# Kernel optimization log

Hardware: AMD Instinct MI355X
Metric: run time of the kernel (lower is better)

The kernel has to match this reference:

```python
import jax, jax.numpy as jnp
import numpy as np
from jax import lax

NPOINT, RADIUS, NSAMPLE = 1024, 0.2, 32
MLP = [64, 64, 128]
EPS = 1e-5  # BatchNorm eps


def setup_inputs() -> dict:
    key = jax.random.key(0)
    ks = jax.random.split(key, 16)
    B, N, D = 16, 4096, 64
    inp = {
        "xyz": jax.random.uniform(ks[0], (B, 3, N), jnp.float32),   # points in unit cube
        "points": jax.random.normal(ks[1], (B, D, N), jnp.float32),  # per-point features
    }
    chans = [3 + D] + MLP  # grouped_xyz_norm (3) concat features (D)
    for i in range(3):
        ci, co = chans[i], chans[i + 1]
        inp[f"W{i}"] = jax.random.normal(ks[2 + 4 * i], (co, ci), jnp.float32) * (1.0 / np.sqrt(ci))
        inp[f"b{i}"] = jnp.zeros((co,), jnp.float32)
        inp[f"g{i}"] = jnp.ones((co,), jnp.float32)    # BN gamma
        inp[f"be{i}"] = jnp.zeros((co,), jnp.float32)  # BN beta
    return inp


def _fps(xyz, npoint):
    # xyz: [B,N,3] -> sampled indices [B,npoint]. Sequential farthest-point sampling.
    B, N, _ = xyz.shape

    def step(carry, _):
        distance, farthest = carry
        centroid = jnp.take_along_axis(xyz, farthest[:, None, None], axis=1)  # [B,1,3]
        d = jnp.sum((xyz - centroid) ** 2, -1)                                # [B,N]
        distance = jnp.minimum(distance, d)
        return (distance, jnp.argmax(distance, -1)), farthest

    init = (jnp.full((B, N), 1e10, xyz.dtype), jnp.zeros((B,), jnp.int32))
    _, idx = lax.scan(step, init, None, length=npoint)
    return idx.T  # [B, npoint]


def _index_points(pts, idx):
    # pts [B,N,C], idx [B,...] int -> [B,...,C]  (batched gather)
    return jax.vmap(lambda p, i: p[i])(pts, idx)


def _ball_query(radius, nsample, xyz, new_xyz):
    # xyz [B,N,3], new_xyz [B,S,3] -> group_idx [B,S,nsample]
    B, N, _ = xyz.shape
    sqr = (jnp.sum(new_xyz ** 2, -1)[:, :, None]
           + jnp.sum(xyz ** 2, -1)[:, None, :]
           - 2.0 * jnp.einsum('bsc,bnc->bsn', new_xyz, xyz))  # [B,S,N]
    # NB: source assigns N-1 (not N) to out-of-radius points; the == N fixup is a no-op,
    # kept here for faithfulness.
    gi = jnp.where(sqr > radius ** 2, N - 1, jnp.arange(N, dtype=jnp.int32)[None, None, :])
    gi = jnp.sort(gi, axis=-1)[:, :, :nsample]
    first = gi[:, :, :1]
    return jnp.where(gi == N, first, gi)


def _forward(xyz, points, params):
    xyzT = jnp.transpose(xyz, (0, 2, 1))    # [B,N,3]
    ptsT = jnp.transpose(points, (0, 2, 1))  # [B,N,D]
    B, N, _ = xyzT.shape
    fps_idx = _fps(xyzT, NPOINT)                              # [B,S]
    new_xyz = _index_points(xyzT, fps_idx)                    # [B,S,3]
    idx = _ball_query(RADIUS, NSAMPLE, xyzT, new_xyz)         # [B,S,K]
    grouped_xyz = _index_points(xyzT, idx) - new_xyz[:, :, None, :]  # [B,S,K,3]
    grouped_pts = _index_points(ptsT, idx)                    # [B,S,K,D]
    feat = jnp.concatenate([grouped_xyz, grouped_pts], -1)    # [B,S,K,3+D]
    x = jnp.transpose(feat, (0, 3, 2, 1))                     # [B,C,K,S]
    for (W, b, g, be) in params:
        x = jnp.einsum('bcks,oc->boks', x, W) + b[None, :, None, None]  # 1x1 conv
        mean = jnp.mean(x, axis=(0, 2, 3), keepdims=True)   # BN (training-mode batch stats)
        var = jnp.var(x, axis=(0, 2, 3), keepdims=True)
        x = (x - mean) / jnp.sqrt(var + EPS) * g[None, :, None, None] + be[None, :, None, None]
        x = jax.nn.relu(x)
    new_points = jnp.max(x, axis=2)                           # [B, mlp[-1], S]
    return jnp.transpose(new_xyz, (0, 2, 1)), new_points


def reference(xyz, points, W0, b0, g0, be0, W1, b1, g1, be1, W2, b2, g2, be2):
    params = [(W0, b0, g0, be0), (W1, b1, g1, be1), (W2, b2, g2, be2)]
    return _forward(xyz, points, params)
```

## Files before the change

### kernel.cpp

```cpp
#include <hip/hip_runtime.h>
#include <cstdint>
#include <cstddef>

#define BB 16
#define NN 4096
#define SS 1024
#define KK 32
#define MROWS (BB*SS*KK)
#define EPSV 1e-5f
#define OUT_OFF1 (BB*3*SS)

static constexpr size_t OFF_XYZT   = 0;
static constexpr size_t OFF_NEWXYZ = OFF_XYZT   + (size_t)BB*NN*16;
static constexpr size_t OFF_BALL   = OFF_NEWXYZ + (size_t)BB*SS*16;
static constexpr size_t OFF_STATS  = OFF_BALL   + (size_t)MROWS*4;
static constexpr size_t OFF_PROG   = OFF_STATS  + 2048;
static constexpr size_t OFF_PT     = OFF_PROG   + 256;
static constexpr size_t OFF_Y      = OFF_PT     + (size_t)BB*NN*64*4;
static constexpr size_t OFF_YMAX   = OFF_Y      + (size_t)MROWS*64*4;
static constexpr size_t OFF_YMIN   = OFF_YMAX   + (size_t)BB*SS*128*4;

__device__ __forceinline__ float sq3(float x, float y, float z) {
  return __fadd_rn(__fadd_rn(__fmul_rn(x,x), __fmul_rn(y,y)), __fmul_rn(z,z));
}

template<int CTRL>
__device__ __forceinline__ unsigned long long dpp_max_u64(unsigned long long k) {
  int lo = (int)(unsigned)k;
  int hi = (int)(unsigned)(k >> 32);
  unsigned olo = (unsigned)__builtin_amdgcn_update_dpp(0, lo, CTRL, 0xf, 0xf, true);
  unsigned ohi = (unsigned)__builtin_amdgcn_update_dpp(0, hi, CTRL, 0xf, 0xf, true);
  unsigned long long o = ((unsigned long long)ohi << 32) | (unsigned long long)olo;
  return o > k ? o : k;
}

__global__ __launch_bounds__(256) void fps_trans_ball(const float* __restrict__ xyz,
                                                      const float* __restrict__ pts,
                                                      float4* __restrict__ xyzt,
                                                      float* __restrict__ pt,
                                                      float4* __restrict__ newxyz,
                                                      int* __restrict__ prog,
                                                      int* __restrict__ ball,
                                                      float* __restrict__ out) {
  __shared__ float sx[NN], sy[NN], sz[NN];
  __shared__ unsigned long long red[2][4];
  __shared__ float tl[64*65];
  int t = threadIdx.x;

  if (blockIdx.x >= 1040) {
    int lane = t & 63, wv = t >> 6;
    int base = (blockIdx.x - 1040)*4;
    int bs = base + wv;
    int b = bs >> 10;
    int need = (base & (SS-1)) + 4;
    if (t == 0) {
      while (__hip_atomic_load(&prog[b], __ATOMIC_ACQUIRE, __HIP_MEMORY_SCOPE_AGENT) < need)
        __builtin_amdgcn_s_sleep(64);
    }
    __syncthreads();
    const float* xb = xyz + (size_t)b*3*NN;
    float4 c = newxyz[bs];
    float sumS = sq3(c.x, c.y, c.z);
    int count = 0;
    for (int ch = 0; ch < NN/64; ++ch) {
      int n = ch*64 + lane;
      float nx = xb[n], ny = xb[NN+n], nz = xb[2*NN+n];
      float sumN = sq3(nx, ny, nz);
      float dt   = __fadd_rn(__fadd_rn(__fmul_rn(c.x,nx), __fmul_rn(c.y,ny)), __fmul_rn(c.z,nz));
      float sqr  = __fsub_rn(__fadd_rn(sumS, sumN), __fmul_rn(2.0f, dt));
      bool isin = !(sqr > 0.04f);
      unsigned long long mask = __ballot(isin);
      int pos = count + (int)__popcll(mask & ((1ull << lane) - 1ull));
      if (isin && pos < KK) ball[(size_t)bs*KK + pos] = n;
      count += (int)__popcll(mask);
      if (count >= KK) break;
    }
    if (count < KK && lane >= count && lane < KK) ball[(size_t)bs*KK + lane] = NN-1;
    return;
  }

  if (blockIdx.x >= 16) {
    int k = blockIdx.x - 16;
    int b = k >> 6, n0 = (k & 63) * 64;
    int ln = t & 63, hi = t >> 6;
#pragma unroll
    for (int i = 0; i < 16; ++i) {
      int c = 4*i + hi;
      tl[c*65 + ln] = pts[((size_t)b*64 + c)*NN + n0 + ln];
    }
    if (t < 64) {
      int n = n0 + t;
      const float* xb = xyz + (size_t)b*3*NN;
      xyzt[(size_t)b*NN + n] = make_float4(xb[n], xb[NN+n], xb[2*NN+n], 0.f);
    }
    __syncthreads();
#pragma unroll
    for (int i = 0; i < 16; ++i) {
      int nn = hi + 4*i;
      pt[((size_t)b*NN + n0 + nn)*64 + ln] = tl[ln*65 + nn];
    }
    return;
  }

  int b = blockIdx.x;
  int lane = t & 63, wv = t >> 6;
  const float* xb = xyz + (size_t)b*3*NN;
  float px[16], py[16], pz[16], dd[16];
#pragma unroll
  for (int j = 0; j < 16; ++j) {
    int n = t + 256*j;
    px[j] = xb[n]; py[j] = xb[NN+n]; pz[j] = xb[2*NN+n];
    sx[n] = px[j]; sy[n] = py[j]; sz[n] = pz[j];
    dd[j] = 1e10f;
  }
  int f = 0;
  float mcx = 0.f, mcy = 0.f, mcz = 0.f;
  __syncthreads();
  for (int i = 0; i < SS; ++i) {
    float cx = sx[f], cy = sy[f], cz = sz[f];
    if (t == (i & 31)) { mcx = cx; mcy = cy; mcz = cz; }
    if ((i & 31) == 31) {
      if (t < 32) {
        int ci = i - 31 + t;
        newxyz[b*SS + ci] = make_float4(mcx, mcy, mcz, 0.f);
        out[(size_t)b*3*SS + ci]        = mcx;
        out[(size_t)b*3*SS + SS + ci]   = mcy;
        out[(size_t)b*3*SS + 2*SS + ci] = mcz;
      }
      if (t == 0)
        __hip_atomic_store(&prog[b], i+1, __ATOMIC_RELEASE, __HIP_MEMORY_SCOPE_AGENT);
    }
    if (i == SS-1) break;
    unsigned long long key[16];
#pragma unroll
    for (int j = 0; j < 16; ++j) {
      float dx = __fsub_rn(px[j], cx);
      float dy = __fsub_rn(py[j], cy);
      float dz = __fsub_rn(pz[j], cz);
      float d  = sq3(dx, dy, dz);
      float nd = dd[j] < d ? dd[j] : d;
      dd[j] = nd;
      key[j] = (((unsigned long long)__float_as_uint(nd)) << 32)
             | (unsigned)(NN-1 - (t + 256*j));
    }
#pragma unroll
    for (int w = 8; w >= 1; w >>= 1)
#pragma unroll
      for (int q = 0; q < w; ++q)
        key[q] = key[q] > key[q+w] ? key[q] : key[q+w];
    unsigned long long bk = key[0];
    bk = dpp_max_u64<0x111>(bk);
    bk = dpp_max_u64<0x112>(bk);
    bk = dpp_max_u64<0x114>(bk);
    bk = dpp_max_u64<0x118>(bk);
    bk = dpp_max_u64<0x142>(bk);
    bk = dpp_max_u64<0x143>(bk);
    if (lane == 63) red[i&1][wv] = bk;
    __syncthreads();
    unsigned long long best = red[i&1][0];
#pragma unroll
    for (int w = 1; w < 4; ++w) { unsigned long long v = red[i&1][w]; if (v > best) best = v; }
    f = (NN-1) - (int)(best & 0xffffffffull);
  }
}

template<int MODE, int CO>
__global__ __launch_bounds__(256) void conv_kernel(
    const float* xin, const float4* __restrict__ xyzt, const float4* __restrict__ newxyz,
    const int* __restrict__ ball, const float* __restrict__ W, const float* __restrict__ bias,
    const float* __restrict__ statsPrev, const float* __restrict__ gPrev,
    const float* __restrict__ bePrev, float* yout, float* __restrict__ statsOut,
    float* __restrict__ ymax, float* __restrict__ ymin) {
  constexpr int NC = CO/16;
  constexpr int CR = (MODE == 0) ? 68 : 64;
  constexpr int C4N = CR/4;
  __shared__ float4 Ws4[CR*CO/4];
  __shared__ float4 Xs4[128*17];
  __shared__ float scIn[64], shIn[64];
  float* Ws = (float*)Ws4;

  int t = threadIdx.x;
  int tc = t & 15;
  int wv = t >> 6;
  int trs = (t >> 4) & 3;
  if constexpr (MODE >= 1) {
    if (t < 64) {
      float mean = statsPrev[t] * (1.0f/MROWS);
      float var  = statsPrev[64+t] * (1.0f/MROWS) - mean*mean;
      float inv  = 1.0f / sqrtf(var + EPSV);
      float sc   = gPrev[t] * inv;
      scIn[t] = sc; shIn[t] = bePrev[t] - mean*sc;
    }
  }
  for (int idx = t; idx < CR*CO; idx += 256) {
    int cc = idx / CO, o = idx % CO;
    float v = 0.f;
    if constexpr (MODE == 0) {
      if (cc < 67) v = W[o*67 + (cc < 64 ? cc+3 : cc-64)];
    } else {
      if (cc < 64) v = W[o*64 + cc];
    }
    Ws[cc*CO + o] = v;
  }
  float bj[NC], accS[NC], accQ[NC];
#pragma unroll
  for (int j = 0; j < NC; ++j) { bj[j] = bias[tc*NC + j]; accS[j] = 0.f; accQ[j] = 0.f; }
  __syncthreads();

  for (int tile = blockIdx.x; tile < MROWS/128; tile += gridDim.x) {
    if constexpr (MODE == 0) {
      int rr = t >> 1, p = t & 1;
      int r = tile*128 + rr;
      int n = ball[r];
      int bb2 = r >> 15;
      const float4* src = (const float4*)(xin + ((size_t)(bb2*NN + n))*64) + 8*p;
#pragma unroll
      for (int jj = 0; jj < 8; ++jj) Xs4[rr*17 + 8*p + jj] = src[jj];
      if (p == 0) {
        float4 pz = xyzt[bb2*NN + n];
        float4 q  = newxyz[r >> 5];
        float* X = (float*)Xs4;
        X[rr*68 + 64] = pz.x - q.x;
        X[rr*68 + 65] = pz.y - q.y;
        X[rr*68 + 66] = pz.z - q.z;
        X[rr*68 + 67] = 0.f;
      }
    } else {
      const float4* src = (const float4*)(xin + (size_t)tile*128*64);
#pragma unroll
      for (int k = 0; k < 8; ++k) {
        int idx = t + 256*k;
        int row = idx >> 4, c4 = idx & 15;
        float4 v = src[idx];
        int c = 4*c4;
        v.x = fmaxf(0.f, fmaf(v.x, scIn[c+0], shIn[c+0]));
        v.y = fmaxf(0.f, fmaf(v.y, scIn[c+1], shIn[c+1]));
        v.z = fmaxf(0.f, fmaf(v.z, scIn[c+2], shIn[c+2]));
        v.w = fmaxf(0.f, fmaf(v.w, scIn[c+3], shIn[c+3]));
        Xs4[row*17 + c4] = v;
      }
    }
    __syncthreads();

    float acc[8][NC];
#pragma unroll
    for (int i = 0; i < 8; ++i)
#pragma unroll
      for (int j = 0; j < NC; ++j) acc[i][j] = bj[j];

    for (int c4 = 0; c4 < C4N; ++c4) {
      float4 a[8];
#pragma unroll
      for (int i = 0; i < 8; ++i) a[i] = Xs4[(32*wv + trs + 4*i)*17 + c4];
      float4 w[4][NC/4];
#pragma unroll
      for (int cc = 0; cc < 4; ++cc)
#pragma unroll
        for (int q = 0; q < NC/4; ++q)
          w[cc][q] = Ws4[(4*c4 + cc)*(CO/4) + tc*(NC/4) + q];
#pragma unroll
      for (int cc = 0; cc < 4; ++cc) {
#pragma unroll
        for (int i = 0; i < 8; ++i) {
          float av = (cc==0) ? a[i].x : (cc==1) ? a[i].y : (cc==2) ? a[i].z : a[i].w;
#pragma unroll
          for (int q = 0; q < NC/4; ++q) {
            acc[i][4*q+0] = fmaf(av, w[cc][q].x, acc[i][4*q+0]);
            acc[i][4*q+1] = fmaf(av, w[cc][q].y, acc[i][4*q+1]);
            acc[i][4*q+2] = fmaf(av, w[cc][q].z, acc[i][4*q+2]);
            acc[i][4*q+3] = fmaf(av, w[cc][q].w, acc[i][4*q+3]);
          }
        }
      }
    }

    if constexpr (MODE <= 1) {
#pragma unroll
      for (int i = 0; i < 8; ++i) {
        size_t rw = (size_t)tile*128 + 32*wv + trs + 4*i;
        float4 v = make_float4(acc[i][0], acc[i][1], acc[i][2], acc[i][3]);
        ((float4*)(yout + rw*64))[tc] = v;
      }
    }
#pragma unroll
    for (int i = 0; i < 8; ++i)
#pragma unroll
      for (int j = 0; j < NC; ++j) {
        float v = acc[i][j];
        accS[j] += v;
        accQ[j] = fmaf(v, v, accQ[j]);
      }

    if constexpr (MODE == 2) {
      float vmx[NC], vmn[NC];
#pragma unroll
      for (int j = 0; j < NC; ++j) {
        float mx = acc[0][j], mn = acc[0][j];
#pragma unroll
        for (int i = 1; i < 8; ++i) { mx = fmaxf(mx, acc[i][j]); mn = fminf(mn, acc[i][j]); }
        vmx[j] = mx; vmn[j] = mn;
      }
#pragma unroll
      for (int m = 16; m <= 32; m <<= 1)
#pragma unroll
        for (int j = 0; j < NC; ++j) {
          vmx[j] = fmaxf(vmx[j], __shfl_xor(vmx[j], m, 64));
          vmn[j] = fminf(vmn[j], __shfl_xor(vmn[j], m, 64));
        }
      if ((t & 63) < 16) {
        size_t gg = (size_t)tile*4 + wv;
        ((float4*)(ymax + gg*128 + 8*tc))[0] = make_float4(vmx[0], vmx[1], vmx[2], vmx[3]);
        ((float4*)(ymax + gg*128 + 8*tc))[1] = make_float4(vmx[4], vmx[5], vmx[6], vmx[7]);
        ((float4*)(ymin + gg*128 + 8*tc))[0] = make_float4(vmn[0], vmn[1], vmn[2], vmn[3]);
        ((float4*)(ymin + gg*128 + 8*tc))[1] = make_float4(vmn[4], vmn[5], vmn[6], vmn[7]);
      }
    }
    __syncthreads();
  }

  float* scratch = (float*)Xs4;
  if (t < 2*CO) scratch[t] = 0.f;
  __syncthreads();
#pragma unroll
  for (int j = 0; j < NC; ++j) {
    atomicAdd(&scratch[tc*NC + j], accS[j]);
    atomicAdd(&scratch[CO + tc*NC + j], accQ[j]);
  }
  __syncthreads();
  if (t < 2*CO) atomicAdd(&statsOut[t], scratch[t]);
}

__global__ __launch_bounds__(256) void final_kernel(const float4* __restrict__ ymax4,
                                                    const float4* __restrict__ ymin4,
                                                    const float* __restrict__ stats2,
                                                    const float* __restrict__ g2,
                                                    const float* __restrict__ be2,
                                                    float* __restrict__ out) {
  __shared__ float sc3[128], sh3[128];
  __shared__ float tile[64*129];
  int t = threadIdx.x;
  if (t < 128) {
    float mean = stats2[t] * (1.0f/MROWS);
    float var  = stats2[128+t] * (1.0f/MROWS) - mean*mean;
    float sc   = g2[t] / sqrtf(var + EPSV);
    sc3[t] = sc; sh3[t] = be2[t] - mean*sc;
  }
  __syncthreads();
  int b = blockIdx.x, s0 = blockIdx.y*64;
#pragma unroll
  for (int pass = 0; pass < 8; ++pass) {
    int srow = pass*8 + (t >> 5);
    int o4 = (t & 31)*4;
    size_t base = (size_t)(b*SS + s0 + srow)*32 + (t & 31);
    float4 vx = ymax4[base], vn = ymin4[base];
#pragma unroll
    for (int e = 0; e < 4; ++e) {
      int o = o4 + e;
      float sc = sc3[o];
      float v = sc > 0.f ? ((const float*)&vx)[e] : ((const float*)&vn)[e];
      tile[srow*129 + o] = fmaxf(0.f, fmaf(v, sc, sh3[o]));
    }
  }
  __syncthreads();
  int s = t & 63;
  size_t obase = (size_t)OUT_OFF1 + (size_t)b*128*SS + s0 + s;
#pragma unroll
  for (int oi = 0; oi < 32; ++oi) {
    int o = (t >> 6) + 4*oi;
    out[obase + (size_t)o*SS] = tile[s*129 + o];
  }
}

extern "C" void kernel_launch(void* const* d_in, const int* in_sizes, int n_in,
                              void* d_out, int out_size, void* d_ws, size_t ws_size,
                              hipStream_t stream) {
  const float* xyz = (const float*)d_in[0];
  const float* pts = (const float*)d_in[1];
  const float* W0  = (const float*)d_in[2];
  const float* b0  = (const float*)d_in[3];
  const float* g0  = (const float*)d_in[4];
  const float* be0 = (const float*)d_in[5];
  const float* W1  = (const float*)d_in[6];
  const float* b1  = (const float*)d_in[7];
  const float* g1  = (const float*)d_in[8];
  const float* be1 = (const float*)d_in[9];
  const float* W2  = (const float*)d_in[10];
  const float* b2  = (const float*)d_in[11];
  const float* g2  = (const float*)d_in[12];
  const float* be2 = (const float*)d_in[13];
  float* out = (float*)d_out;
  char* ws = (char*)d_ws;

  float4* xyzt   = (float4*)(ws + OFF_XYZT);
  float4* newxyz = (float4*)(ws + OFF_NEWXYZ);
  int*    ball   = (int*)(ws + OFF_BALL);
  float*  stats  = (float*)(ws + OFF_STATS);
  int*    prog   = (int*)(ws + OFF_PROG);
  float*  pt     = (float*)(ws + OFF_PT);
  float*  y      = (float*)(ws + OFF_Y);
  float*  ymax   = (float*)(ws + OFF_YMAX);
  float*  ymin   = (float*)(ws + OFF_YMIN);

  hipMemsetAsync(stats, 0, 2048 + 256, stream);
  fps_trans_ball<<<16 + BB*(NN/64) + BB*SS/4, 256, 0, stream>>>(
      xyz, pts, xyzt, pt, newxyz, prog, ball, out);
  conv_kernel<0,64><<<1024, 256, 0, stream>>>(pt, xyzt, newxyz, ball, W0, b0,
      nullptr, nullptr, nullptr, y, stats, nullptr, nullptr);
  conv_kernel<1,64><<<1024, 256, 0, stream>>>(y, nullptr, nullptr, nullptr, W1, b1,
      stats, g0, be0, y, stats+128, nullptr, nullptr);
  conv_kernel<2,128><<<1024, 256, 0, stream>>>(y, nullptr, nullptr, nullptr, W2, b2,
      stats+128, g1, be1, nullptr, stats+256, ymax, ymin);
  final_kernel<<<dim3(BB, SS/64), 256, 0, stream>>>((const float4*)ymax, (const float4*)ymin,
      stats+256, g2, be2, out);
}
```

Baseline: 1.186 ms.

## Fuse ball query with first conv layer inside FPS kernel, split transpose out

Moves the point-feature transpose into its own kernel and fuses ball query with the first 1x1 conv (gather, matmul, BN stats) in the FPS-overlapped kernel. Ball indices stay in shared memory instead of going through a global buffer, and one kernel launch plus its global round trip are removed. Layer-0 work now overlaps with the sequential FPS blocks. FPS shared coordinates are packed into a float4 layout. The risks are a larger shared-memory footprint, which lowers occupancy, and a BN-stats atomic per block.

```diff
diff --git a/kernel.cpp b/kernel.cpp
--- a/kernel.cpp
+++ b/kernel.cpp
@@ -34,30 +34,70 @@
   return o > k ? o : k;
 }
 
-__global__ __launch_bounds__(256) void fps_trans_ball(const float* __restrict__ xyz,
-                                                      const float* __restrict__ pts,
-                                                      float4* __restrict__ xyzt,
-                                                      float* __restrict__ pt,
+__global__ __launch_bounds__(256) void trans_kernel(const float* __restrict__ xyz,
+                                                    const float* __restrict__ pts,
+                                                    float4* __restrict__ xyzt,
+                                                    float* __restrict__ pt) {
+  __shared__ float tl[64*65];
+  int t = threadIdx.x;
+  int k = blockIdx.x;
+  int b = k >> 6, n0 = (k & 63) * 64;
+  int ln = t & 63, hi = t >> 6;
+#pragma unroll
+  for (int i = 0; i < 16; ++i) {
+    int c = 4*i + hi;
+    tl[c*65 + ln] = pts[((size_t)b*64 + c)*NN + n0 + ln];
+  }
+  if (t < 64) {
+    int n = n0 + t;
+    const float* xb = xyz + (size_t)b*3*NN;
+    xyzt[(size_t)b*NN + n] = make_float4(xb[n], xb[NN+n], xb[2*NN+n], 0.f);
+  }
+  __syncthreads();
+#pragma unroll
+  for (int i = 0; i < 16; ++i) {
+    int nn = hi + 4*i;
+    pt[((size_t)b*NN + n0 + nn)*64 + ln] = tl[ln*65 + nn];
+  }
+}
+
+__global__ __launch_bounds__(256) void fps_ball_conv0(const float* __restrict__ xyz,
+                                                      const float4* __restrict__ xyzt,
+                                                      const float* __restrict__ pt,
                                                       float4* __restrict__ newxyz,
                                                       int* __restrict__ prog,
-                                                      int* __restrict__ ball,
-                                                      float* __restrict__ out) {
-  __shared__ float sx[NN], sy[NN], sz[NN];
-  __shared__ unsigned long long red[2][4];
-  __shared__ float tl[64*65];
+                                                      float* __restrict__ out,
+                                                      const float* __restrict__ W0,
+                                                      const float* __restrict__ bias0,
+                                                      float* __restrict__ y,
+                                                      float* __restrict__ stats0) {
+  __shared__ __align__(16) char smem[65600];
   int t = threadIdx.x;
 
-  if (blockIdx.x >= 1040) {
+  if (blockIdx.x >= 16) {
+    float4* Ws4  = (float4*)smem;
+    float*  Ws   = (float*)Ws4;
+    float4* Xs4  = (float4*)(smem + 17408);
+    int*    bidx = (int*)(smem + 52224);
     int lane = t & 63, wv = t >> 6;
-    int base = (blockIdx.x - 1040)*4;
+    int base = (blockIdx.x - 16)*4;
     int bs = base + wv;
     int b = bs >> 10;
+
+    for (int idx = t; idx < 68*64; idx += 256) {
+      int cc = idx >> 6, o = idx & 63;
+      float v = 0.f;
+      if (cc < 67) v = W0[o*67 + (cc < 64 ? cc+3 : cc-64)];
+      Ws[(cc << 6) + o] = v;
+    }
+
     int need = (base & (SS-1)) + 4;
     if (t == 0) {
       while (__hip_atomic_load(&prog[b], __ATOMIC_ACQUIRE, __HIP_MEMORY_SCOPE_AGENT) < need)
         __builtin_amdgcn_s_sleep(64);
     }
     __syncthreads();
+
     const float* xb = xyz + (size_t)b*3*NN;
     float4 c = newxyz[bs];
     float sumS = sq3(c.x, c.y, c.z);
@@ -71,37 +111,92 @@
       bool isin = !(sqr > 0.04f);
       unsigned long long mask = __ballot(isin);
       int pos = count + (int)__popcll(mask & ((1ull << lane) - 1ull));
-      if (isin && pos < KK) ball[(size_t)bs*KK + pos] = n;
+      if (isin && pos < KK) bidx[(wv << 5) + pos] = n;
       count += (int)__popcll(mask);
       if (count >= KK) break;
     }
-    if (count < KK && lane >= count && lane < KK) ball[(size_t)bs*KK + lane] = NN-1;
+    if (count < KK && lane >= count && lane < KK) bidx[(wv << 5) + lane] = NN-1;
+    __syncthreads();
+
+    {
+      int rr = t >> 1, p = t & 1;
+      int n = bidx[rr];
+      const float4* src = (const float4*)(pt + ((size_t)(b*NN + n))*64) + 8*p;
+#pragma unroll
+      for (int jj = 0; jj < 8; ++jj) Xs4[rr*17 + 8*p + jj] = src[jj];
+      if (p == 0) {
+        float4 pz = xyzt[b*NN + n];
+        float4 q  = newxyz[base + (rr >> 5)];
+        float* X = (float*)Xs4;
+        X[rr*68 + 64] = pz.x - q.x;
+        X[rr*68 + 65] = pz.y - q.y;
+        X[rr*68 + 66] = pz.z - q.z;
+        X[rr*68 + 67] = 0.f;
+      }
+    }
+    __syncthreads();
+
+    int tc = t & 15, trs = (t >> 4) & 3;
+    float accS[4], accQ[4];
+#pragma unroll
+    for (int j = 0; j < 4; ++j) { accS[j] = 0.f; accQ[j] = 0.f; }
+
+    float acc[8][4];
+#pragma unroll
+    for (int i = 0; i < 8; ++i)
+#pragma unroll
+      for (int j = 0; j < 4; ++j) acc[i][j] = bias0[tc*4 + j];
+
+    for (int c4 = 0; c4 < 17; ++c4) {
+      float4 a[8];
+#pragma unroll
+      for (int i = 0; i < 8; ++i) a[i] = Xs4[(32*wv + trs + 4*i)*17 + c4];
+      float4 w[4];
+#pragma unroll
+      for (int cc = 0; cc < 4; ++cc) w[cc] = Ws4[(4*c4 + cc)*16 + tc];
+#pragma unroll
+      for (int cc = 0; cc < 4; ++cc) {
+#pragma unroll
+        for (int i = 0; i < 8; ++i) {
+          float av = (cc==0) ? a[i].x : (cc==1) ? a[i].y : (cc==2) ? a[i].z : a[i].w;
+          acc[i][0] = fmaf(av, w[cc].x, acc[i][0]);
+          acc[i][1] = fmaf(av, w[cc].y, acc[i][1]);
+          acc[i][2] = fmaf(av, w[cc].z, acc[i][2]);
+          acc[i][3] = fmaf(av, w[cc].w, acc[i][3]);
+        }
+      }
+    }
+
+#pragma unroll
+    for (int i = 0; i < 8; ++i) {
+      size_t rw = (size_t)base*32 + 32*wv + trs + 4*i;
+      ((float4*)(y + rw*64))[tc] = make_float4(acc[i][0], acc[i][1], acc[i][2], acc[i][3]);
+    }
+#pragma unroll
+    for (int i = 0; i < 8; ++i)
+#pragma unroll
+      for (int j = 0; j < 4; ++j) {
+        float v = acc[i][j];
+        accS[j] += v;
+        accQ[j] = fmaf(v, v, accQ[j]);
+      }
+
+    __syncthreads();
+    float* scratch = (float*)Xs4;
+    if (t < 128) scratch[t] = 0.f;
+    __syncthreads();
+#pragma unroll
+    for (int j = 0; j < 4; ++j) {
+      atomicAdd(&scratch[tc*4 + j], accS[j]);
+      atomicAdd(&scratch[64 + tc*4 + j], accQ[j]);
+    }
+    __syncthreads();
+    if (t < 128) atomicAdd(&stats0[t], scratch[t]);
     return;
   }
 
-  if (blockIdx.x >= 16) {
-    int k = blockIdx.x - 16;
-    int b = k >> 6, n0 = (k & 63) * 64;
-    int ln = t & 63, hi = t >> 6;
-#pragma unroll
-    for (int i = 0; i < 16; ++i) {
-      int c = 4*i + hi;
-      tl[c*65 + ln] = pts[((size_t)b*64 + c)*NN + n0 + ln];
-    }
-    if (t < 64) {
-      int n = n0 + t;
-      const float* xb = xyz + (size_t)b*3*NN;
-      xyzt[(size_t)b*NN + n] = make_float4(xb[n], xb[NN+n], xb[2*NN+n], 0.f);
-    }
-    __syncthreads();
-#pragma unroll
-    for (int i = 0; i < 16; ++i) {
-      int nn = hi + 4*i;
-      pt[((size_t)b*NN + n0 + nn)*64 + ln] = tl[ln*65 + nn];
-    }
-    return;
-  }
-
+  float4* sxyz = (float4*)smem;
+  unsigned long long (*red)[4] = (unsigned long long (*)[4])(smem + 65536);
   int b = blockIdx.x;
   int lane = t & 63, wv = t >> 6;
   const float* xb = xyz + (size_t)b*3*NN;
@@ -110,14 +205,15 @@
   for (int j = 0; j < 16; ++j) {
     int n = t + 256*j;
     px[j] = xb[n]; py[j] = xb[NN+n]; pz[j] = xb[2*NN+n];
-    sx[n] = px[j]; sy[n] = py[j]; sz[n] = pz[j];
+    sxyz[n] = make_float4(px[j], py[j], pz[j], 0.f);
     dd[j] = 1e10f;
   }
   int f = 0;
   float mcx = 0.f, mcy = 0.f, mcz = 0.f;
   __syncthreads();
   for (int i = 0; i < SS; ++i) {
-    float cx = sx[f], cy = sy[f], cz = sz[f];
+    float4 cc4 = sxyz[f];
+    float cx = cc4.x, cy = cc4.y, cz = cc4.z;
     if (t == (i & 31)) { mcx = cx; mcy = cy; mcz = cz; }
     if ((i & 31) == 31) {
       if (t < 32) {
@@ -166,13 +262,12 @@
 
 template<int MODE, int CO>
 __global__ __launch_bounds__(256) void conv_kernel(
-    const float* xin, const float4* __restrict__ xyzt, const float4* __restrict__ newxyz,
-    const int* __restrict__ ball, const float* __restrict__ W, const float* __restrict__ bias,
+    const float* xin, const float* __restrict__ W, const float* __restrict__ bias,
     const float* __restrict__ statsPrev, const float* __restrict__ gPrev,
     const float* __restrict__ bePrev, float* yout, float* __restrict__ statsOut,
     float* __restrict__ ymax, float* __restrict__ ymin) {
   constexpr int NC = CO/16;
-  constexpr int CR = (MODE == 0) ? 68 : 64;
+  constexpr int CR = 64;
   constexpr int C4N = CR/4;
   __shared__ float4 Ws4[CR*CO/4];
   __shared__ float4 Xs4[128*17];
@@ -183,24 +278,16 @@
   int tc = t & 15;
   int wv = t >> 6;
   int trs = (t >> 4) & 3;
-  if constexpr (MODE >= 1) {
-    if (t < 64) {
-      float mean = statsPrev[t] * (1.0f/MROWS);
-      float var  = statsPrev[64+t] * (1.0f/MROWS) - mean*mean;
-      float inv  = 1.0f / sqrtf(var + EPSV);
-      float sc   = gPrev[t] * inv;
-      scIn[t] = sc; shIn[t] = bePrev[t] - mean*sc;
-    }
+  if (t < 64) {
+    float mean = statsPrev[t] * (1.0f/MROWS);
+    float var  = statsPrev[64+t] * (1.0f/MROWS) - mean*mean;
+    float inv  = 1.0f / sqrtf(var + EPSV);
+    float sc   = gPrev[t] * inv;
+    scIn[t] = sc; shIn[t] = bePrev[t] - mean*sc;
   }
   for (int idx = t; idx < CR*CO; idx += 256) {
     int cc = idx / CO, o = idx % CO;
-    float v = 0.f;
-    if constexpr (MODE == 0) {
-      if (cc < 67) v = W[o*67 + (cc < 64 ? cc+3 : cc-64)];
-    } else {
-      if (cc < 64) v = W[o*64 + cc];
-    }
-    Ws[cc*CO + o] = v;
+    Ws[cc*CO + o] = W[o*64 + cc];
   }
   float bj[NC], accS[NC], accQ[NC];
 #pragma unroll
@@ -208,24 +295,7 @@
   __syncthreads();
 
   for (int tile = blockIdx.x; tile < MROWS/128; tile += gridDim.x) {
-    if constexpr (MODE == 0) {
-      int rr = t >> 1, p = t & 1;
-      int r = tile*128 + rr;
-      int n = ball[r];
-      int bb2 = r >> 15;
-      const float4* src = (const float4*)(xin + ((size_t)(bb2*NN + n))*64) + 8*p;
-#pragma unroll
-      for (int jj = 0; jj < 8; ++jj) Xs4[rr*17 + 8*p + jj] = src[jj];
-      if (p == 0) {
-        float4 pz = xyzt[bb2*NN + n];
-        float4 q  = newxyz[r >> 5];
-        float* X = (float*)Xs4;
-        X[rr*68 + 64] = pz.x - q.x;
-        X[rr*68 + 65] = pz.y - q.y;
-        X[rr*68 + 66] = pz.z - q.z;
-        X[rr*68 + 67] = 0.f;
-      }
-    } else {
+    {
       const float4* src = (const float4*)(xin + (size_t)tile*128*64);
 #pragma unroll
       for (int k = 0; k < 8; ++k) {
@@ -393,7 +463,6 @@
 
   float4* xyzt   = (float4*)(ws + OFF_XYZT);
   float4* newxyz = (float4*)(ws + OFF_NEWXYZ);
-  int*    ball   = (int*)(ws + OFF_BALL);
   float*  stats  = (float*)(ws + OFF_STATS);
   int*    prog   = (int*)(ws + OFF_PROG);
   float*  pt     = (float*)(ws + OFF_PT);
@@ -402,13 +471,12 @@
   float*  ymin   = (float*)(ws + OFF_YMIN);
 
   hipMemsetAsync(stats, 0, 2048 + 256, stream);
-  fps_trans_ball<<<16 + BB*(NN/64) + BB*SS/4, 256, 0, stream>>>(
-      xyz, pts, xyzt, pt, newxyz, prog, ball, out);
-  conv_kernel<0,64><<<1024, 256, 0, stream>>>(pt, xyzt, newxyz, ball, W0, b0,
-      nullptr, nullptr, nullptr, y, stats, nullptr, nullptr);
-  conv_kernel<1,64><<<1024, 256, 0, stream>>>(y, nullptr, nullptr, nullptr, W1, b1,
+  trans_kernel<<<BB*(NN/64), 256, 0, stream>>>(xyz, pts, xyzt, pt);
+  fps_ball_conv0<<<16 + BB*SS/4, 256, 0, stream>>>(
+      xyz, (const float4*)xyzt, pt, newxyz, prog, out, W0, b0, y, stats);
+  conv_kernel<1,64><<<1024, 256, 0, stream>>>(y, W1, b1,
       stats, g0, be0, y, stats+128, nullptr, nullptr);
-  conv_kernel<2,128><<<1024, 256, 0, stream>>>(y, nullptr, nullptr, nullptr, W2, b2,
+  conv_kernel<2,128><<<1024, 256, 0, stream>>>(y, W2, b2,
       stats+128, g1, be1, nullptr, stats+256, ymax, ymin);
   final_kernel<<<dim3(BB, SS/64), 256, 0, stream>>>((const float4*)ymax, (const float4*)ymin,
       stats+256, g2, be2, out);
```

Measured after the change: 1.154 ms (median of 2 runs). 1.03x faster.
